# Performance work log

Measured on AMD Instinct MI355X. Metric: run time of the kernel, lower is better.

The kernel has to match this reference:

```python
import jax, jax.numpy as jnp
import numpy as np

N_LOW = 50000
N_HIGH = 200000
E = 1000000       # number of (i, j, k) triplets from the radius search
K = 27            # 3x3x3 voxel kernel cells
C_IN = 128
C_OUT = 128


def setup_inputs() -> dict:
    key = jax.random.key(0)
    k0, k1, k2, k3, k4, k5 = jax.random.split(key, 6)
    x_low = jax.random.normal(k0, (N_LOW, C_IN), dtype=jnp.float32)
    # PointConv3d weight: one [C_OUT, C_IN] matrix per kernel cell, kaiming-ish scale
    weight = jax.random.normal(k1, (K, C_OUT, C_IN), dtype=jnp.float32) * (1.0 / np.sqrt(C_IN))
    bias = jax.random.normal(k2, (C_OUT,), dtype=jnp.float32) * 0.01
    i_high = jax.random.randint(k3, (E,), 0, N_HIGH, dtype=jnp.int32)
    j_low = jax.random.randint(k4, (E,), 0, N_LOW, dtype=jnp.int32)
    k_cell = jax.random.randint(k5, (E,), 0, K, dtype=jnp.int32)
    return {"x_low": x_low, "weight": weight, "bias": bias,
            "i_high": i_high, "j_low": j_low, "k": k_cell, "n_high": N_HIGH}


def reference(x_low, weight, bias, i_high, j_low, k, n_high):
    # Sparse point convolution: out[i] += weight[k] @ x_low[j], then + bias.
    # Efficient form: transform every low-res point by all K kernel matrices once
    # (dense GEMM), then gather the (j, k) entry per triplet and scatter-add by i.
    y = jnp.einsum('nc,koc->nko', x_low, weight)       # [N_low, K, C_out]
    msg = y[j_low, k]                                  # [E, C_out] gather
    out = jnp.zeros((n_high, weight.shape[1]), dtype=x_low.dtype)
    out = out.at[i_high].add(msg)                      # scatter-add to high-res points
    return out + bias
```

## Files before the change

kernel.cpp:

```cpp
#include <hip/hip_runtime.h>

typedef _Float16 half8 __attribute__((ext_vector_type(8)));
typedef _Float16 half4v __attribute__((ext_vector_type(4)));
typedef _Float16 half2v __attribute__((ext_vector_type(2)));
typedef float f32x4 __attribute__((ext_vector_type(4)));

#define CAP 32
#define OVF_MAX 4096


__global__ void zero_ints(int* __restrict__ p, int n) {
    int i = blockIdx.x * blockDim.x + threadIdx.x;
    if (i < n) p[i] = 0;
}

__global__ void init_bias(float* __restrict__ out, const float* __restrict__ bias, int n4) {
    int i = blockIdx.x * blockDim.x + threadIdx.x;
    if (i >= n4) return;
    reinterpret_cast<float4*>(out)[i] = reinterpret_cast<const float4*>(bias)[i & 31];
}

__global__ __launch_bounds__(256) void cvt_mask(
    const float* __restrict__ x, const float* __restrict__ w,
    const float* __restrict__ bias,
    _Float16* __restrict__ Xh, _Float16* __restrict__ Wh,
    float* __restrict__ biasPerm, _Float16* __restrict__ Yz,
    const int* __restrict__ ih, const int* __restrict__ jl,
    const int* __restrict__ kc,
    unsigned char* __restrict__ maskB,
    int* __restrict__ counts, int* __restrict__ bucket,
    int* __restrict__ ovf_cnt, int* __restrict__ ovf_list,
    int Mpad, int ldY, int xv4, int xt4, int w4, int E, int eg) {
    int i = blockIdx.x * blockDim.x + threadIdx.x;
    if (i < xt4) {
        float4 v = (i < xv4) ? reinterpret_cast<const float4*>(x)[i]
                             : make_float4(0.f, 0.f, 0.f, 0.f);
        half4v h; h[0]=(_Float16)v.x; h[1]=(_Float16)v.y; h[2]=(_Float16)v.z; h[3]=(_Float16)v.w;
        reinterpret_cast<half4v*>(Xh)[i] = h;
    } else if (i < xt4 + w4) {
        int j = i - xt4;
        float4 v = reinterpret_cast<const float4*>(w)[j];
        half4v h; h[0]=(_Float16)v.x; h[1]=(_Float16)v.y; h[2]=(_Float16)v.z; h[3]=(_Float16)v.w;
        reinterpret_cast<half4v*>(Wh)[j] = h;
    } else if (i < xt4 + w4 + 32) {
        int j2 = i - xt4 - w4;
        int wn = j2 >> 4, mrow = j2 & 15;
        float4 v;
        v.x = bias[wn * 64 + 0 * 16 + mrow];
        v.y = bias[wn * 64 + 1 * 16 + mrow];
        v.z = bias[wn * 64 + 2 * 16 + mrow];
        v.w = bias[wn * 64 + 3 * 16 + mrow];
        reinterpret_cast<float4*>(biasPerm)[j2] = v;
    } else if (i < xt4 + w4 + 48) {
        int t = i - xt4 - w4 - 32;
        reinterpret_cast<int4*>(Yz)[t] = make_int4(0, 0, 0, 0);
    } else {
        int e = i - (xt4 + w4 + 48);
        if (e < E) {
            int j = jl[e], kk = kc[e];
            maskB[(size_t)kk * Mpad + j] = 1;
            if (e >= eg) {
                int ii = ih[e];
                int off = j * ldY + kk * 128;
                int pos = atomicAdd(&counts[ii], 1);
                if (pos < CAP) {
                    bucket[(size_t)ii * CAP + pos] = off;
                } else {
                    int o = atomicAdd(ovf_cnt, 1);
                    if (o < OVF_MAX) { ovf_list[2 * o] = ii; ovf_list[2 * o + 1] = off; }
                }
            }
        }
    }
}

__global__ __launch_bounds__(256) void gemm_xw(
    const _Float16* __restrict__ Xh,
    const _Float16* __restrict__ Wh,
    _Float16* __restrict__ Y,
    const unsigned char* __restrict__ maskB,
    int Mpad, int ldY,
    const int* __restrict__ ih, const int* __restrict__ jl,
    const int* __restrict__ kc,
    int* __restrict__ counts, int* __restrict__ bucket,
    int* __restrict__ ovf_cnt, int* __restrict__ ovf_list, int eg) {
    __shared__ ushort sA[128 * 128];
    __shared__ ushort sB[128 * 128];
    const int tid = threadIdx.x;
    const int m0 = blockIdx.x * 128;
    const int kc0 = blockIdx.y * 3;
    const ushort* Ag = (const ushort*)Xh + (size_t)m0 * 128;

#pragma unroll
    for (int it = 0; it < 8; ++it) {
        int p = it * 256 + tid;
        int row = p >> 4, cpos = p & 15;
        int csrc = cpos ^ (row & 15);
        __builtin_amdgcn_global_load_lds(
            (const __attribute__((address_space(1))) void*)(Ag + row * 128 + csrc * 8),
            (__attribute__((address_space(3))) void*)(&sA[row * 128 + cpos * 8]), 16, 0, 0);
    }
    {
        const ushort* Bg = (const ushort*)Wh + (size_t)kc0 * 128 * 128;
#pragma unroll
        for (int it = 0; it < 8; ++it) {
            int p = it * 256 + tid;
            int row = p >> 4, cpos = p & 15;
            int csrc = cpos ^ (row & 15);
            __builtin_amdgcn_global_load_lds(
                (const __attribute__((address_space(1))) void*)(Bg + row * 128 + csrc * 8),
                (__attribute__((address_space(3))) void*)(&sB[row * 128 + cpos * 8]), 16, 0, 0);
        }
    }
    __builtin_amdgcn_sched_barrier(0);

    const int bid = blockIdx.y * gridDim.x + blockIdx.x;
    const bool hasE = (bid * 256) < eg;
    int i0 = 0, off0 = 0, pos0 = CAP;
    if (hasE) {
        int e = bid * 256 + tid;
        i0 = ih[e];
        off0 = jl[e] * ldY + kc[e] * 128;
        pos0 = atomicAdd(&counts[i0], 1);
        __builtin_amdgcn_sched_barrier(0);
        asm volatile("s_waitcnt vmcnt(4)" ::: "memory");
    } else {
        __builtin_amdgcn_sched_barrier(0);
        asm volatile("s_waitcnt vmcnt(0)" ::: "memory");
    }
    __builtin_amdgcn_sched_barrier(0);
    __builtin_amdgcn_s_barrier();
    __builtin_amdgcn_sched_barrier(0);

    const int lane = tid & 63;
    const int wid = tid >> 6;
    const int wm = wid & 1, wn = wid >> 1;
    const int mrow = lane & 15;
    const int g = lane >> 4;

    for (int kk = 0; kk < 3; ++kk) {
        f32x4 acc[4][4] = {};
#pragma unroll
        for (int kb = 0; kb < 4; ++kb) {
            half8 af[4], bf[4];
#pragma unroll
            for (int t = 0; t < 4; ++t) {
                int cpos8 = ((kb * 4 + g) ^ mrow) * 8;
                int ra = wm * 64 + t * 16 + mrow;
                af[t] = *reinterpret_cast<const half8*>(&sA[ra * 128 + cpos8]);
                int rb = wn * 64 + t * 16 + mrow;
                bf[t] = *reinterpret_cast<const half8*>(&sB[rb * 128 + cpos8]);
            }
#pragma unroll
            for (int mt = 0; mt < 4; ++mt)
#pragma unroll
                for (int nt = 0; nt < 4; ++nt)
                    acc[mt][nt] = __builtin_amdgcn_mfma_f32_16x16x32_f16(
                        af[mt], bf[nt], acc[mt][nt], 0, 0, 0);
        }
        if (kk < 2) {
            __builtin_amdgcn_s_barrier();
            __builtin_amdgcn_sched_barrier(0);
            const ushort* Bg = (const ushort*)Wh + (size_t)(kc0 + kk + 1) * 128 * 128;
#pragma unroll
            for (int it = 0; it < 8; ++it) {
                int p = it * 256 + tid;
                int row = p >> 4, cpos = p & 15;
                int csrc = cpos ^ (row & 15);
                __builtin_amdgcn_global_load_lds(
                    (const __attribute__((address_space(1))) void*)(Bg + row * 128 + csrc * 8),
                    (__attribute__((address_space(3))) void*)(&sB[row * 128 + cpos * 8]), 16, 0, 0);
            }
        }
        if (kk == 0 && hasE) {
            if (pos0 < CAP) {
                bucket[(size_t)i0 * CAP + pos0] = off0;
            } else {
                int o = atomicAdd(ovf_cnt, 1);
                if (o < OVF_MAX) { ovf_list[2 * o] = i0; ovf_list[2 * o + 1] = off0; }
            }
        }
        const unsigned char* mBp = maskB + (size_t)(kc0 + kk) * Mpad + m0 + wm * 64;
        _Float16* Yt = Y + (size_t)m0 * ldY + (kc0 + kk) * 128 + wn * 64 + mrow * 4;
#pragma unroll
        for (int mt = 0; mt < 4; ++mt) {
            unsigned mw = *reinterpret_cast<const unsigned*>(mBp + mt * 16 + g * 4);
            if (mw) {
#pragma unroll
                for (int r = 0; r < 4; ++r) {
                    if ((mw >> (8 * r)) & 0xFFu) {
                        int row = wm * 64 + mt * 16 + g * 4 + r;
                        half4v hv;
#pragma unroll
                        for (int nt = 0; nt < 4; ++nt) hv[nt] = (_Float16)acc[mt][nt][r];
                        *reinterpret_cast<half4v*>(Yt + (size_t)row * ldY) = hv;
                    }
                }
            }
        }
        if (kk < 2) {
            __builtin_amdgcn_s_waitcnt(0);
            __syncthreads();
        }
    }
}

__global__ __launch_bounds__(256) void gather_out(
    const _Float16* __restrict__ Y, const int* __restrict__ counts,
    const int* __restrict__ bucket, const float* __restrict__ biasPerm,
    float* __restrict__ out, int Nhigh, int zoff) {
    int wave = (blockIdx.x * blockDim.x + threadIdx.x) >> 6;
    int lane = threadIdx.x & 63;
    int p = lane >> 4;
    int sub = lane & 15;
    int i = wave * 4 + p;
    bool act = i < Nhigh;
    int iC = act ? i : 0;
    int nb = counts[iC];
    if (nb > CAP) nb = CAP;
    const int* bk = bucket + (size_t)iC * CAP;
    int offsA = bk[sub];
    int offsB = bk[sub + 16];
    float4 b0 = reinterpret_cast<const float4*>(biasPerm)[sub * 2];
    float4 b1 = reinterpret_cast<const float4*>(biasPerm)[sub * 2 + 1];
    float acc[8] = {b0.x, b0.y, b0.z, b0.w, b1.x, b1.y, b1.z, b1.w};

    int nmax = nb;
    nmax = max(nmax, __shfl_xor(nmax, 16));
    nmax = max(nmax, __shfl_xor(nmax, 32));

    for (int e0 = 0; e0 < nmax; e0 += 8) {
#pragma unroll
        for (int u = 0; u < 8; ++u) {
            int e = e0 + u;
            int off = (e < 16) ? __shfl(offsA, p * 16 + (e & 15))
                               : __shfl(offsB, p * 16 + (e & 15));
            bool valid = act && (e < nb);
            off = valid ? off : zoff;
            half8 h = *reinterpret_cast<const half8*>(Y + (size_t)off + sub * 8);
#pragma unroll
            for (int t = 0; t < 8; ++t) acc[t] += (float)h[t];
        }
    }
    if (act) {
        float* op = out + (size_t)i * 128;
        int obase = (sub >> 3) * 64 + (sub & 7) * 2;
#pragma unroll
        for (int t = 0; t < 8; ++t)
            op[obase + (t & 3) * 16 + (t >> 2)] = acc[t];
    }
}

__global__ void apply_overflow(const int* __restrict__ ovf_cnt, const int* __restrict__ ovf_list,
                               const _Float16* __restrict__ Y, float* __restrict__ out) {
    int n = *ovf_cnt;
    if (n > OVF_MAX) n = OVF_MAX;
    int lane = threadIdx.x & 63;
    int w = threadIdx.x >> 6;
    int o0p = 2 * lane, o1p = 2 * lane + 1;
    int o0 = (o0p >> 6) * 64 + (o0p & 3) * 16 + ((o0p >> 2) & 15);
    int o1 = (o1p >> 6) * 64 + (o1p & 3) * 16 + ((o1p >> 2) & 15);
    for (int o = w; o < n; o += 4) {
        int i = ovf_list[2 * o], off = ovf_list[2 * o + 1];
        half2v h = *reinterpret_cast<const half2v*>(Y + (size_t)off + lane * 2);
        float* dst = out + (size_t)i * 128;
        unsafeAtomicAdd(dst + o0, (float)h[0]);
        unsafeAtomicAdd(dst + o1, (float)h[1]);
    }
}

__global__ void fallback_edge(const float* __restrict__ x, const float* __restrict__ w,
                              const int* __restrict__ ih, const int* __restrict__ jl,
                              const int* __restrict__ kc, float* __restrict__ out, int E) {
    int e = blockIdx.x;
    if (e >= E) return;
    int lane = threadIdx.x;
    int i = ih[e], j = jl[e], k = kc[e];
    const float* xr = x + (size_t)j * 128;
    const float* wk = w + (size_t)k * 128 * 128;
    float s0 = 0.f, s1 = 0.f;
    for (int c = 0; c < 128; ++c) {
        float xv = xr[c];
        s0 += wk[(size_t)lane * 128 + c] * xv;
        s1 += wk[(size_t)(lane + 64) * 128 + c] * xv;
    }
    unsafeAtomicAdd(&out[(size_t)i * 128 + lane], s0);
    unsafeAtomicAdd(&out[(size_t)i * 128 + 64 + lane], s1);
}

extern "C" void kernel_launch(void* const* d_in, const int* in_sizes, int n_in,
                              void* d_out, int out_size, void* d_ws, size_t ws_size,
                              hipStream_t stream) {
    const float* x    = (const float*)d_in[0];
    const float* w    = (const float*)d_in[1];
    const float* bias = (const float*)d_in[2];
    const int*   ih   = (const int*)d_in[3];
    const int*   jl   = (const int*)d_in[4];
    const int*   kc   = (const int*)d_in[5];
    float* out = (float*)d_out;

    const int C = 128;
    const int Nlow = in_sizes[0] / C;
    const int K = in_sizes[1] / (C * C);
    const int E = in_sizes[3];
    const int ldY = K * C;
    const int Nhigh = out_size / C;

    const int mtiles = (Nlow + 127) / 128;
    const int Mpad = mtiles * 128;

    size_t off = 0;
    auto alloc = [&](size_t bytes) { size_t o = off; off = (off + bytes + 255) & ~(size_t)255; return o; };
    size_t xh_off   = alloc((size_t)Mpad * C * 2);
    size_t wh_off   = alloc((size_t)K * C * C * 2);
    size_t bp_off   = alloc((size_t)C * 4);
    size_t cnt_off  = alloc(((size_t)Nhigh + 1) * 4 + (size_t)Mpad * K);
    size_t ovl_off  = alloc((size_t)OVF_MAX * 2 * 4);
    size_t bkt_off  = alloc((size_t)Nhigh * CAP * 4);
    size_t y_off    = alloc(((size_t)Mpad * ldY + C) * 2);
    size_t need_sort = off;

    _Float16* Xh = (_Float16*)((char*)d_ws + xh_off);
    _Float16* Wh = (_Float16*)((char*)d_ws + wh_off);
    float* biasPerm = (float*)((char*)d_ws + bp_off);
    int* counts  = (int*)((char*)d_ws + cnt_off);
    int* ovf_cnt = counts + Nhigh;
    unsigned char* maskB = (unsigned char*)(counts + Nhigh + 1);
    int* ovf_lst = (int*)((char*)d_ws + ovl_off);
    int* bucket  = (int*)((char*)d_ws + bkt_off);
    _Float16* Y  = (_Float16*)((char*)d_ws + y_off);
    const int zoff = Mpad * ldY;

    if (ws_size >= need_sort && (K % 3) == 0) {
        int xv4 = Nlow * C / 4, xt4 = Mpad * C / 4;
        int w4 = K * C * C / 4;
        int nbGemm = mtiles * (K / 3);
        long long cap256 = (long long)nbGemm * 256;
        int eg = (E < cap256) ? (E & ~255) : (int)cap256;

        int nz = Nhigh + 1 + (Mpad * K) / 4;
        zero_ints<<<(nz + 255) / 256, 256, 0, stream>>>(counts, nz);

        int totalCvt = xt4 + w4 + 48 + E;
        cvt_mask<<<(totalCvt + 255) / 256, 256, 0, stream>>>(
            x, w, bias, Xh, Wh, biasPerm, Y + (size_t)zoff,
            ih, jl, kc, maskB, counts, bucket, ovf_cnt, ovf_lst,
            Mpad, ldY, xv4, xt4, w4, E, eg);

        gemm_xw<<<dim3(mtiles, K / 3), 256, 0, stream>>>(
            Xh, Wh, Y, maskB, Mpad, ldY,
            ih, jl, kc, counts, bucket, ovf_cnt, ovf_lst, eg);

        gather_out<<<(Nhigh + 15) / 16, 256, 0, stream>>>(
            Y, counts, bucket, biasPerm, out, Nhigh, zoff);
        apply_overflow<<<1, 256, 0, stream>>>(ovf_cnt, ovf_lst, Y, out);
    } else {
        int n4out = out_size / 4;
        init_bias<<<(n4out + 255) / 256, 256, 0, stream>>>(out, bias, n4out);
        fallback_edge<<<E, 64, 0, stream>>>(x, w, ih, jl, kc, out, E);
    }
}
```

Measured before the change: 350.3 us.

## Remap GEMM blocks per XCD, prefetch masks, branchless stores, relax waitcnt

The GEMM grid becomes 1D and block IDs are remapped so that consecutive work (all K-groups of one m-tile) lands on the same XCD, which is meant to improve L2 reuse of the X tile. Mask words for all three kernel cells are loaded up front, and the masked output stores become branchless: unused rows are written to a dummy buffer instead of being skipped. The per-iteration full s_waitcnt(0) is replaced with partial vmcnt waits so stores can overlap the next B-tile load. MFMA sections also get raised wave priority. The branchless stores issue every row write, which adds store traffic to the dump buffer, and the hand-counted vmcnt values are fragile.

```diff
diff --git a/kernel.cpp b/kernel.cpp
--- a/kernel.cpp
+++ b/kernel.cpp
@@ -79,7 +79,8 @@
     const _Float16* __restrict__ Wh,
     _Float16* __restrict__ Y,
     const unsigned char* __restrict__ maskB,
-    int Mpad, int ldY,
+    _Float16* __restrict__ dump,
+    int Mpad, int ldY, int KD,
     const int* __restrict__ ih, const int* __restrict__ jl,
     const int* __restrict__ kc,
     int* __restrict__ counts, int* __restrict__ bucket,
@@ -87,10 +88,46 @@
     __shared__ ushort sA[128 * 128];
     __shared__ ushort sB[128 * 128];
     const int tid = threadIdx.x;
-    const int m0 = blockIdx.x * 128;
-    const int kc0 = blockIdx.y * 3;
+
+    const int nwg = gridDim.x;
+    const int bid = blockIdx.x;
+    {
+    }
+    const int q = nwg >> 3, r = nwg & 7;
+    const int xcd = bid & 7, idx = bid >> 3;
+    const int wg = (xcd < r) ? xcd * (q + 1) + idx
+                             : r * (q + 1) + (xcd - r) * q + idx;
+    const int mtile = wg / KD;
+    const int ky = wg - mtile * KD;
+    const int m0 = mtile * 128;
+    const int kc0 = ky * 3;
+
+    const int lane = tid & 63;
+    const int wid = tid >> 6;
+    const int wm = wid & 1, wn = wid >> 1;
+    const int mrow = lane & 15;
+    const int g = lane >> 4;
+
+    const bool hasE = (bid * 256) < eg;
+    int i0 = 0, off0 = 0, pos0 = CAP;
+    if (hasE) {
+        int e = bid * 256 + tid;
+        i0 = ih[e];
+        off0 = jl[e] * ldY + kc[e] * 128;
+    }
+    unsigned mwv0[4], mwv1[4], mwv2[4];
+    {
+        const unsigned char* mb = maskB + (size_t)kc0 * Mpad + m0 + wm * 64 + g * 4;
+#pragma unroll
+        for (int mt = 0; mt < 4; ++mt) {
+            mwv0[mt] = *reinterpret_cast<const unsigned*>(mb + mt * 16);
+            mwv1[mt] = *reinterpret_cast<const unsigned*>(mb + Mpad + mt * 16);
+            mwv2[mt] = *reinterpret_cast<const unsigned*>(mb + 2 * Mpad + mt * 16);
+        }
+    }
+    __builtin_amdgcn_sched_barrier(0);
+
     const ushort* Ag = (const ushort*)Xh + (size_t)m0 * 128;
-
 #pragma unroll
     for (int it = 0; it < 8; ++it) {
         int p = it * 256 + tid;
@@ -114,16 +151,10 @@
     }
     __builtin_amdgcn_sched_barrier(0);
 
-    const int bid = blockIdx.y * gridDim.x + blockIdx.x;
-    const bool hasE = (bid * 256) < eg;
-    int i0 = 0, off0 = 0, pos0 = CAP;
     if (hasE) {
-        int e = bid * 256 + tid;
-        i0 = ih[e];
-        off0 = jl[e] * ldY + kc[e] * 128;
         pos0 = atomicAdd(&counts[i0], 1);
         __builtin_amdgcn_sched_barrier(0);
-        asm volatile("s_waitcnt vmcnt(4)" ::: "memory");
+        asm volatile("s_waitcnt vmcnt(1)" ::: "memory");
     } else {
         __builtin_amdgcn_sched_barrier(0);
         asm volatile("s_waitcnt vmcnt(0)" ::: "memory");
@@ -132,14 +163,10 @@
     __builtin_amdgcn_s_barrier();
     __builtin_amdgcn_sched_barrier(0);
 
-    const int lane = tid & 63;
-    const int wid = tid >> 6;
-    const int wm = wid & 1, wn = wid >> 1;
-    const int mrow = lane & 15;
-    const int g = lane >> 4;
-
+#pragma unroll
     for (int kk = 0; kk < 3; ++kk) {
         f32x4 acc[4][4] = {};
+        __builtin_amdgcn_s_setprio(1);
 #pragma unroll
         for (int kb = 0; kb < 4; ++kb) {
             half8 af[4], bf[4];
@@ -158,6 +185,9 @@
                     acc[mt][nt] = __builtin_amdgcn_mfma_f32_16x16x32_f16(
                         af[mt], bf[nt], acc[mt][nt], 0, 0, 0);
         }
+        __builtin_amdgcn_s_setprio(0);
+        __builtin_amdgcn_sched_barrier(0);
+
         if (kk < 2) {
             __builtin_amdgcn_s_barrier();
             __builtin_amdgcn_sched_barrier(0);
@@ -171,6 +201,7 @@
                     (const __attribute__((address_space(1))) void*)(Bg + row * 128 + csrc * 8),
                     (__attribute__((address_space(3))) void*)(&sB[row * 128 + cpos * 8]), 16, 0, 0);
             }
+            __builtin_amdgcn_sched_barrier(0);
         }
         if (kk == 0 && hasE) {
             if (pos0 < CAP) {
@@ -180,27 +211,34 @@
                 if (o < OVF_MAX) { ovf_list[2 * o] = i0; ovf_list[2 * o + 1] = off0; }
             }
         }
-        const unsigned char* mBp = maskB + (size_t)(kc0 + kk) * Mpad + m0 + wm * 64;
         _Float16* Yt = Y + (size_t)m0 * ldY + (kc0 + kk) * 128 + wn * 64 + mrow * 4;
+        _Float16* dumpL = dump + lane * 4;
 #pragma unroll
         for (int mt = 0; mt < 4; ++mt) {
-            unsigned mw = *reinterpret_cast<const unsigned*>(mBp + mt * 16 + g * 4);
-            if (mw) {
-#pragma unroll
-                for (int r = 0; r < 4; ++r) {
-                    if ((mw >> (8 * r)) & 0xFFu) {
-                        int row = wm * 64 + mt * 16 + g * 4 + r;
-                        half4v hv;
-#pragma unroll
-                        for (int nt = 0; nt < 4; ++nt) hv[nt] = (_Float16)acc[mt][nt][r];
-                        *reinterpret_cast<half4v*>(Yt + (size_t)row * ldY) = hv;
-                    }
-                }
+            unsigned mw = (kk == 0) ? mwv0[mt] : (kk == 1) ? mwv1[mt] : mwv2[mt];
+#pragma unroll
+            for (int r = 0; r < 4; ++r) {
+                int row = wm * 64 + mt * 16 + g * 4 + r;
+                half4v hv;
+#pragma unroll
+                for (int nt = 0; nt < 4; ++nt) hv[nt] = (_Float16)acc[mt][nt][r];
+                bool use = (mw >> (8 * r)) & 1u;
+                _Float16* dst = use ? (Yt + (size_t)row * ldY) : dumpL;
+                *reinterpret_cast<half4v*>(dst) = hv;
             }
         }
-        if (kk < 2) {
-            __builtin_amdgcn_s_waitcnt(0);
-            __syncthreads();
+        __builtin_amdgcn_sched_barrier(0);
+        if (kk == 0) {
+            if (hasE) { asm volatile("s_waitcnt vmcnt(17)" ::: "memory"); }
+            else      { asm volatile("s_waitcnt vmcnt(16)" ::: "memory"); }
+            __builtin_amdgcn_sched_barrier(0);
+            __builtin_amdgcn_s_barrier();
+            __builtin_amdgcn_sched_barrier(0);
+        } else if (kk == 1) {
+            asm volatile("s_waitcnt vmcnt(16)" ::: "memory");
+            __builtin_amdgcn_sched_barrier(0);
+            __builtin_amdgcn_s_barrier();
+            __builtin_amdgcn_sched_barrier(0);
         }
     }
 }
@@ -317,6 +355,7 @@
     size_t cnt_off  = alloc(((size_t)Nhigh + 1) * 4 + (size_t)Mpad * K);
     size_t ovl_off  = alloc((size_t)OVF_MAX * 2 * 4);
     size_t bkt_off  = alloc((size_t)Nhigh * CAP * 4);
+    size_t dmp_off  = alloc(512);
     size_t y_off    = alloc(((size_t)Mpad * ldY + C) * 2);
     size_t need_sort = off;
 
@@ -328,14 +367,16 @@
     unsigned char* maskB = (unsigned char*)(counts + Nhigh + 1);
     int* ovf_lst = (int*)((char*)d_ws + ovl_off);
     int* bucket  = (int*)((char*)d_ws + bkt_off);
+    _Float16* dump = (_Float16*)((char*)d_ws + dmp_off);
     _Float16* Y  = (_Float16*)((char*)d_ws + y_off);
     const int zoff = Mpad * ldY;
 
     if (ws_size >= need_sort && (K % 3) == 0) {
         int xv4 = Nlow * C / 4, xt4 = Mpad * C / 4;
         int w4 = K * C * C / 4;
-        int nbGemm = mtiles * (K / 3);
-        long long cap256 = (long long)nbGemm * 256;
+        int KD = K / 3;
+        int nwg = mtiles * KD;
+        long long cap256 = (long long)nwg * 256;
         int eg = (E < cap256) ? (E & ~255) : (int)cap256;
 
         int nz = Nhigh + 1 + (Mpad * K) / 4;
@@ -347,8 +388,8 @@
             ih, jl, kc, maskB, counts, bucket, ovf_cnt, ovf_lst,
             Mpad, ldY, xv4, xt4, w4, E, eg);
 
-        gemm_xw<<<dim3(mtiles, K / 3), 256, 0, stream>>>(
-            Xh, Wh, Y, maskB, Mpad, ldY,
+        gemm_xw<<<nwg, 256, 0, stream>>>(
+            Xh, Wh, Y, maskB, dump, Mpad, ldY, KD,
             ih, jl, kc, counts, bucket, ovf_cnt, ovf_lst, eg);
 
         gather_out<<<(Nhigh + 15) / 16, 256, 0, stream>>>(
```

New measurement: 357.2 us. About the same (+2.0%).
